# Kernel tuning notes

Hardware: AMD Instinct MI355X
Metric: run time of the kernel (lower is better)

The kernel has to match this reference:

```python
import jax, jax.numpy as jnp
import numpy as np

B, S, I, H = 128, 1024, 512, 1024


def setup_inputs() -> dict:
    key = jax.random.key(0)
    k0, k1, k2, k3, k4, k5 = jax.random.split(key, 6)
    bound = 1.0 / np.sqrt(H)  # PyTorch LSTMCell init range
    sequence = jax.random.normal(k0, (B, S, I), dtype=jnp.float32)
    input_length = jax.random.randint(k1, (B,), 1, S + 1)  # at least length 1
    W_ih = jax.random.uniform(k2, (4 * H, I), minval=-bound, maxval=bound, dtype=jnp.float32)
    W_hh = jax.random.uniform(k3, (4 * H, H), minval=-bound, maxval=bound, dtype=jnp.float32)
    b_ih = jax.random.uniform(k4, (4 * H,), minval=-bound, maxval=bound, dtype=jnp.float32)
    b_hh = jax.random.uniform(k5, (4 * H,), minval=-bound, maxval=bound, dtype=jnp.float32)
    return {"sequence": sequence, "input_length": input_length,
            "W_ih": W_ih, "W_hh": W_hh, "b_ih": b_ih, "b_hh": b_hh}


def reference(sequence, input_length, W_ih, W_hh, b_ih, b_hh):
    # LSTM acceptor: run LSTMCell over time, return hidden state at t = len-1.
    batch, seq_len, _ = sequence.shape
    hidden = W_hh.shape[1]
    h0 = jnp.zeros((batch, hidden), sequence.dtype)
    c0 = jnp.zeros((batch, hidden), sequence.dtype)
    last0 = jnp.zeros((batch, hidden), sequence.dtype)
    last_step = input_length - 1  # [B]

    def step(carry, xs):
        h, c, last = carry
        x_t, t = xs  # x_t: [B, I]
        gates = x_t @ W_ih.T + b_ih + h @ W_hh.T + b_hh  # [B, 4H]
        i_g, f_g, g_g, o_g = jnp.split(gates, 4, axis=-1)  # PyTorch order i,f,g,o
        c = jax.nn.sigmoid(f_g) * c + jax.nn.sigmoid(i_g) * jnp.tanh(g_g)
        h = jax.nn.sigmoid(o_g) * jnp.tanh(c)
        last = jnp.where((t == last_step)[:, None], h, last)
        return (h, c, last), None

    xs = (jnp.swapaxes(sequence, 0, 1), jnp.arange(seq_len, dtype=input_length.dtype))
    (h, c, last), _ = jax.lax.scan(step, (h0, c0, last0), xs)
    return last
```

## Files before the change

### kernel.cpp

```cpp
#include <hip/hip_runtime.h>
#include <hip/hip_bf16.h>
#include <math.h>

#define B_   128
#define S_   1024
#define I_   512
#define H_   1024
#define KC   1536
#define NWG  256
#define NTHR 512
#define LDA  1544

typedef __bf16 v8bf __attribute__((ext_vector_type(8)));
typedef float  v4f  __attribute__((ext_vector_type(4)));

__device__ __forceinline__ v8bf cvt8(const float4 a, const float4 b) {
    v8bf r;
    r[0] = (__bf16)a.x; r[1] = (__bf16)a.y; r[2] = (__bf16)a.z; r[3] = (__bf16)a.w;
    r[4] = (__bf16)b.x; r[5] = (__bf16)b.y; r[6] = (__bf16)b.z; r[7] = (__bf16)b.w;
    return r;
}

__device__ __forceinline__ float sigm(float x) { return 1.f / (1.f + __expf(-x)); }
__device__ __forceinline__ float tanh_fast(float x) {
    const float xc = fminf(fmaxf(x, -15.f), 15.f);
    const float e  = __expf(2.f * xc);
    return (e - 1.f) / (e + 1.f);
}

__global__ void lstm_pack(const float* __restrict__ Wih, const float* __restrict__ Whh,
                          __bf16* __restrict__ Wc)
{
    const size_t e = ((size_t)blockIdx.x * 256 + threadIdx.x) * 8;
    const int col = (int)(e / KC);
    const int k   = (int)(e % KC);
    const float4* src = (k < I_) ? (const float4*)&Wih[(size_t)col * I_ + k]
                                 : (const float4*)&Whh[(size_t)col * H_ + (k - I_)];
    const float4 a = src[0], b = src[1];
    *(v8bf*)&Wc[e] = cvt8(a, b);
}

__global__ __launch_bounds__(NTHR, 1) void lstm_persist(
    const float* __restrict__ seq, const int* __restrict__ len,
    const __bf16* __restrict__ Wc,
    const float* __restrict__ bih, const float* __restrict__ bhh,
    float* __restrict__ out, __bf16* __restrict__ hA, __bf16* __restrict__ hB,
    unsigned* __restrict__ cnt)
{
    __shared__ __bf16 Apan[16 * LDA];
    __shared__ float  glds[4][2][16][33];

    const int wg   = blockIdx.x;
    const int bg   = wg & 7;
    const int cg   = wg >> 3;
    const int tid  = threadIdx.x;
    const int lane = tid & 63;
    const int wv   = tid >> 6;
    const int l15  = lane & 15;
    const int q    = lane >> 4;
    const int gate = wv >> 1;
    const int ks   = wv & 1;

    const int n0   = gate * H_ + cg * 32;
    const int col0 = n0 + l15;
    const int col1 = n0 + 16 + l15;

    v8bf wx0[8], wx1[8], wh0[16], wh1[16];
    {
        const __bf16* wr0 = Wc + (size_t)col0 * KC;
        const __bf16* wr1 = Wc + (size_t)col1 * KC;
        const int xo = ks * 256 + q * 8;
        const int ho = I_ + ks * 512 + q * 8;
        #pragma unroll
        for (int j = 0; j < 8; ++j) {
            wx0[j] = *(const v8bf*)(wr0 + xo + j * 32);
            wx1[j] = *(const v8bf*)(wr1 + xo + j * 32);
        }
        #pragma unroll
        for (int j = 0; j < 16; ++j) {
            wh0[j] = *(const v8bf*)(wr0 + ho + j * 32);
            wh1[j] = *(const v8bf*)(wr1 + ho + j * 32);
        }
        #pragma unroll
        for (int j = 0; j < 8; ++j)
            asm volatile("" : "+v"(wx0[j]), "+v"(wx1[j]));
        #pragma unroll
        for (int j = 0; j < 16; ++j)
            asm volatile("" : "+v"(wh0[j]), "+v"(wh1[j]));
    }
    const float b0 = ks ? 0.f : (bih[col0] + bhh[col0]);
    const float b1 = ks ? 0.f : (bih[col1] + bhh[col1]);

    const int cb = tid >> 5;
    const int cc = tid & 31;
    const int gb = bg * 16 + cb;
    const int gc = cg * 32 + cc;
    const int mylen = len[gb];
    float creg = 0.f;

    for (int t = 0; t < S_; ++t) {
        const __bf16* hrd = (t & 1) ? hA : hB;
        __bf16*       hwr = (t & 1) ? hB : hA;

        {
            const float4* xp = (const float4*)&seq[((size_t)gb * S_ + (size_t)t) * I_ + cc * 16];
            v8bf* dx = (v8bf*)&Apan[cb * LDA + cc * 16];
            const float4 x0 = xp[0], x1 = xp[1];
            dx[0] = cvt8(x0, x1);
            const float4 x2 = xp[2], x3 = xp[3];
            dx[1] = cvt8(x2, x3);
        }

        if (t > 0 && tid == 0) {
            const unsigned* c0 = cnt + ((size_t)(t - 1) * 4) * 32 + bg;
            unsigned s;
            do {
                s  = __hip_atomic_load(c0 +  0, __ATOMIC_RELAXED, __HIP_MEMORY_SCOPE_AGENT);
                s += __hip_atomic_load(c0 + 32, __ATOMIC_RELAXED, __HIP_MEMORY_SCOPE_AGENT);
                s += __hip_atomic_load(c0 + 64, __ATOMIC_RELAXED, __HIP_MEMORY_SCOPE_AGENT);
                s += __hip_atomic_load(c0 + 96, __ATOMIC_RELAXED, __HIP_MEMORY_SCOPE_AGENT);
            } while (s < 32u);
        }
        __syncthreads();

        unsigned long long hv8[8];
        {
            const unsigned long long* hs =
                (const unsigned long long*)(hrd + (size_t)(bg * 16) * H_);
            #pragma unroll
            for (int j = 0; j < 8; ++j)
                hv8[j] = __hip_atomic_load(&hs[cb * 256 + cc + 32 * j],
                                           __ATOMIC_RELAXED, __HIP_MEMORY_SCOPE_AGENT);
        }

        v4f acc0 = {0.f, 0.f, 0.f, 0.f};
        v4f acc1 = {0.f, 0.f, 0.f, 0.f};
        {
            const __bf16* ap = &Apan[l15 * LDA + ks * 256 + q * 8];
            #pragma unroll
            for (int j = 0; j < 8; ++j) {
                const v8bf a = *(const v8bf*)(ap + j * 32);
                acc0 = __builtin_amdgcn_mfma_f32_16x16x32_bf16(a, wx0[j], acc0, 0, 0, 0);
                acc1 = __builtin_amdgcn_mfma_f32_16x16x32_bf16(a, wx1[j], acc1, 0, 0, 0);
            }
        }

        #pragma unroll
        for (int j = 0; j < 8; ++j)
            *(unsigned long long*)&Apan[cb * LDA + I_ + 4 * (cc + 32 * j)] = hv8[j];
        __syncthreads();

        {
            const __bf16* ap = &Apan[l15 * LDA + I_ + ks * 512 + q * 8];
            #pragma unroll
            for (int j = 0; j < 16; ++j) {
                const v8bf a = *(const v8bf*)(ap + j * 32);
                acc0 = __builtin_amdgcn_mfma_f32_16x16x32_bf16(a, wh0[j], acc0, 0, 0, 0);
                acc1 = __builtin_amdgcn_mfma_f32_16x16x32_bf16(a, wh1[j], acc1, 0, 0, 0);
            }
        }

        #pragma unroll
        for (int r = 0; r < 4; ++r) {
            glds[gate][ks][q * 4 + r][l15]      = acc0[r] + b0;
            glds[gate][ks][q * 4 + r][16 + l15] = acc1[r] + b1;
        }
        __syncthreads();

        const float ig = glds[0][0][cb][cc] + glds[0][1][cb][cc];
        const float fg = glds[1][0][cb][cc] + glds[1][1][cb][cc];
        const float gg = glds[2][0][cb][cc] + glds[2][1][cb][cc];
        const float og = glds[3][0][cb][cc] + glds[3][1][cb][cc];

        const float cn = sigm(fg) * creg + sigm(ig) * tanh_fast(gg);
        const float hv = sigm(og) * tanh_fast(cn);
        creg = cn;

        const __bf16 hb = (__bf16)hv;
        const unsigned short us = __builtin_bit_cast(unsigned short, hb);
        const unsigned nb = __shfl_xor((unsigned)us, 1);
        if ((lane & 1) == 0) {
            const unsigned pair = (unsigned)us | (nb << 16);
            __hip_atomic_store((unsigned*)&hwr[(size_t)gb * H_ + gc], pair,
                               __ATOMIC_RELAXED, __HIP_MEMORY_SCOPE_AGENT);
        }
        if (t == mylen - 1) out[(size_t)gb * H_ + gc] = hv;

        __syncthreads();
        if (tid == 0)
            __hip_atomic_fetch_add(cnt + ((size_t)t * 4 + (cg & 3)) * 32 + bg, 1u,
                                   __ATOMIC_RELAXED, __HIP_MEMORY_SCOPE_AGENT);
    }
}

extern "C" void kernel_launch(void* const* d_in, const int* in_sizes, int n_in,
                              void* d_out, int out_size, void* d_ws, size_t ws_size,
                              hipStream_t stream) {
    const float* seq = (const float*)d_in[0];
    const int*   len = (const int*)d_in[1];
    const float* Wih = (const float*)d_in[2];
    const float* Whh = (const float*)d_in[3];
    const float* bih = (const float*)d_in[4];
    const float* bhh = (const float*)d_in[5];
    float* out = (float*)d_out;

    char* ws = (char*)d_ws;
    __bf16*   Wc  = (__bf16*)ws;
    __bf16*   hA  = (__bf16*)(ws + 12582912);
    __bf16*   hB  = (__bf16*)(ws + 12845056);
    unsigned* cnt = (unsigned*)(ws + 13107200);

    hipMemsetAsync(hA, 0, 2 * (size_t)B_ * H_ * sizeof(__bf16), stream);
    hipMemsetAsync(cnt, 0, (size_t)S_ * 4 * 32 * sizeof(unsigned), stream);

    lstm_pack<<<dim3(3072), dim3(256), 0, stream>>>(Wih, Whh, Wc);

    void* args[] = {(void*)&seq, (void*)&len, (void*)&Wc, (void*)&bih,
                    (void*)&bhh, (void*)&out, (void*)&hA, (void*)&hB, (void*)&cnt};
    hipError_t e = hipLaunchCooperativeKernel((void*)lstm_persist, dim3(NWG),
                                              dim3(NTHR), args, 0, stream);
    if (e != hipSuccess) {
        lstm_persist<<<dim3(NWG), dim3(NTHR), 0, stream>>>(seq, len, Wc, bih,
                                                           bhh, out, hA, hB, cnt);
    }
}
```

Measured before the change: 3.348 ms.

## Retile persistent LSTM to 32 batch rows by 16 columns and prefetch next x

Each workgroup now covers 32 batch rows and 16 hidden columns per gate instead of 16 by 32. The grid becomes 4 batch groups by 64 column groups, and the per-step barrier counters grow to 8 slots. Each weight register fragment now feeds two MFMAs over two row halves, which halves the weight registers per wave. The next step's input row is prefetched into a double-buffered LDS panel and overlaps with the recurrent MFMAs, taking the x load off the critical path. In exchange each workgroup reads twice as much h from global memory per step, and the barrier wait now polls 64 arrivals from 8 counters.

```diff
diff --git a/kernel.cpp b/kernel.cpp
--- a/kernel.cpp
+++ b/kernel.cpp
@@ -9,10 +9,12 @@
 #define KC   1536
 #define NWG  256
 #define NTHR 512
-#define LDA  1544
+#define XLD  528
+#define HLD  1040
 
 typedef __bf16 v8bf __attribute__((ext_vector_type(8)));
 typedef float  v4f  __attribute__((ext_vector_type(4)));
+typedef unsigned long long ull;
 
 __device__ __forceinline__ v8bf cvt8(const float4 a, const float4 b) {
     v8bf r;
@@ -47,148 +49,163 @@
     float* __restrict__ out, __bf16* __restrict__ hA, __bf16* __restrict__ hB,
     unsigned* __restrict__ cnt)
 {
-    __shared__ __bf16 Apan[16 * LDA];
-    __shared__ float  glds[4][2][16][33];
+    __shared__ __bf16 xpan[2][32 * XLD];
+    __shared__ __bf16 hpan[32 * HLD];
+    __shared__ float  glds[4][2][32][18];
 
     const int wg   = blockIdx.x;
-    const int bg   = wg & 7;
-    const int cg   = wg >> 3;
+    const int bg   = wg & 3;
+    const int cg   = wg >> 2;
     const int tid  = threadIdx.x;
     const int lane = tid & 63;
     const int wv   = tid >> 6;
     const int l15  = lane & 15;
     const int q    = lane >> 4;
-    const int gate = wv >> 1;
+    const int g    = wv >> 1;
     const int ks   = wv & 1;
 
-    const int n0   = gate * H_ + cg * 32;
-    const int col0 = n0 + l15;
-    const int col1 = n0 + 16 + l15;
-
-    v8bf wx0[8], wx1[8], wh0[16], wh1[16];
+    const int col = g * H_ + cg * 16 + l15;
+
+    v8bf w[24];
     {
-        const __bf16* wr0 = Wc + (size_t)col0 * KC;
-        const __bf16* wr1 = Wc + (size_t)col1 * KC;
-        const int xo = ks * 256 + q * 8;
-        const int ho = I_ + ks * 512 + q * 8;
-        #pragma unroll
-        for (int j = 0; j < 8; ++j) {
-            wx0[j] = *(const v8bf*)(wr0 + xo + j * 32);
-            wx1[j] = *(const v8bf*)(wr1 + xo + j * 32);
-        }
-        #pragma unroll
-        for (int j = 0; j < 16; ++j) {
-            wh0[j] = *(const v8bf*)(wr0 + ho + j * 32);
-            wh1[j] = *(const v8bf*)(wr1 + ho + j * 32);
-        }
+        const __bf16* wr = Wc + (size_t)col * KC;
         #pragma unroll
         for (int j = 0; j < 8; ++j)
-            asm volatile("" : "+v"(wx0[j]), "+v"(wx1[j]));
+            w[j] = *(const v8bf*)(wr + ks * 256 + q * 8 + j * 32);
         #pragma unroll
         for (int j = 0; j < 16; ++j)
-            asm volatile("" : "+v"(wh0[j]), "+v"(wh1[j]));
-    }
-    const float b0 = ks ? 0.f : (bih[col0] + bhh[col0]);
-    const float b1 = ks ? 0.f : (bih[col1] + bhh[col1]);
-
-    const int cb = tid >> 5;
-    const int cc = tid & 31;
-    const int gb = bg * 16 + cb;
-    const int gc = cg * 32 + cc;
+            w[8 + j] = *(const v8bf*)(wr + I_ + ks * 512 + q * 8 + j * 32);
+        #pragma unroll
+        for (int j = 0; j < 24; ++j) asm volatile("" : "+v"(w[j]));
+    }
+    const float b0 = ks ? 0.f : (bih[col] + bhh[col]);
+
+    const int cb  = tid >> 4;
+    const int ccc = tid & 15;
+    const int gb  = bg * 32 + cb;
+    const int gc  = cg * 16 + ccc;
     const int mylen = len[gb];
     float creg = 0.f;
 
+    const float* xrow = seq + (size_t)gb * (S_ * I_);
+
+    {
+        const float4* xs = (const float4*)xrow;
+        #pragma unroll
+        for (int jj = 0; jj < 4; ++jj) {
+            const int fi = 2 * ccc + 32 * jj;
+            const float4 a = xs[fi], b = xs[fi + 1];
+            *(v8bf*)&xpan[0][cb * XLD + fi * 4] = cvt8(a, b);
+        }
+    }
+
     for (int t = 0; t < S_; ++t) {
+        const int buf = t & 1;
         const __bf16* hrd = (t & 1) ? hA : hB;
         __bf16*       hwr = (t & 1) ? hB : hA;
 
-        {
-            const float4* xp = (const float4*)&seq[((size_t)gb * S_ + (size_t)t) * I_ + cc * 16];
-            v8bf* dx = (v8bf*)&Apan[cb * LDA + cc * 16];
-            const float4 x0 = xp[0], x1 = xp[1];
-            dx[0] = cvt8(x0, x1);
-            const float4 x2 = xp[2], x3 = xp[3];
-            dx[1] = cvt8(x2, x3);
-        }
-
         if (t > 0 && tid == 0) {
-            const unsigned* c0 = cnt + ((size_t)(t - 1) * 4) * 32 + bg;
+            const unsigned* c0 = cnt + ((size_t)(t - 1) * 8) * 32 + bg;
             unsigned s;
             do {
-                s  = __hip_atomic_load(c0 +  0, __ATOMIC_RELAXED, __HIP_MEMORY_SCOPE_AGENT);
-                s += __hip_atomic_load(c0 + 32, __ATOMIC_RELAXED, __HIP_MEMORY_SCOPE_AGENT);
-                s += __hip_atomic_load(c0 + 64, __ATOMIC_RELAXED, __HIP_MEMORY_SCOPE_AGENT);
-                s += __hip_atomic_load(c0 + 96, __ATOMIC_RELAXED, __HIP_MEMORY_SCOPE_AGENT);
-            } while (s < 32u);
-        }
-        __syncthreads();
-
-        unsigned long long hv8[8];
+                s = 0;
+                #pragma unroll
+                for (int u = 0; u < 8; ++u)
+                    s += __hip_atomic_load(c0 + u * 32, __ATOMIC_RELAXED,
+                                           __HIP_MEMORY_SCOPE_AGENT);
+            } while (s < 64u);
+        }
+        __syncthreads();
+
+        ull hv[16];
         {
-            const unsigned long long* hs =
-                (const unsigned long long*)(hrd + (size_t)(bg * 16) * H_);
-            #pragma unroll
-            for (int j = 0; j < 8; ++j)
-                hv8[j] = __hip_atomic_load(&hs[cb * 256 + cc + 32 * j],
-                                           __ATOMIC_RELAXED, __HIP_MEMORY_SCOPE_AGENT);
+            const ull* hs = (const ull*)(hrd + (size_t)(bg * 32) * H_);
+            #pragma unroll
+            for (int j = 0; j < 16; ++j)
+                hv[j] = __hip_atomic_load(&hs[cb * 256 + ccc + 16 * j],
+                                          __ATOMIC_RELAXED, __HIP_MEMORY_SCOPE_AGENT);
         }
 
         v4f acc0 = {0.f, 0.f, 0.f, 0.f};
         v4f acc1 = {0.f, 0.f, 0.f, 0.f};
         {
-            const __bf16* ap = &Apan[l15 * LDA + ks * 256 + q * 8];
+            const __bf16* ap0 = &xpan[buf][l15 * XLD + ks * 256 + q * 8];
+            const __bf16* ap1 = ap0 + 16 * XLD;
             #pragma unroll
             for (int j = 0; j < 8; ++j) {
-                const v8bf a = *(const v8bf*)(ap + j * 32);
-                acc0 = __builtin_amdgcn_mfma_f32_16x16x32_bf16(a, wx0[j], acc0, 0, 0, 0);
-                acc1 = __builtin_amdgcn_mfma_f32_16x16x32_bf16(a, wx1[j], acc1, 0, 0, 0);
-            }
-        }
-
-        #pragma unroll
-        for (int j = 0; j < 8; ++j)
-            *(unsigned long long*)&Apan[cb * LDA + I_ + 4 * (cc + 32 * j)] = hv8[j];
-        __syncthreads();
+                acc0 = __builtin_amdgcn_mfma_f32_16x16x32_bf16(
+                           *(const v8bf*)(ap0 + j * 32), w[j], acc0, 0, 0, 0);
+                acc1 = __builtin_amdgcn_mfma_f32_16x16x32_bf16(
+                           *(const v8bf*)(ap1 + j * 32), w[j], acc1, 0, 0, 0);
+            }
+        }
+
+        #pragma unroll
+        for (int j = 0; j < 16; ++j)
+            *(ull*)&hpan[cb * HLD + 4 * (ccc + 16 * j)] = hv[j];
+        __syncthreads();
+
+        float4 xf[8];
+        const bool pf = (t + 1 < S_);
+        if (pf) {
+            const float4* xs = (const float4*)(xrow + (size_t)(t + 1) * I_);
+            #pragma unroll
+            for (int jj = 0; jj < 4; ++jj) {
+                const int fi = 2 * ccc + 32 * jj;
+                xf[2 * jj]     = xs[fi];
+                xf[2 * jj + 1] = xs[fi + 1];
+            }
+        }
 
         {
-            const __bf16* ap = &Apan[l15 * LDA + I_ + ks * 512 + q * 8];
+            const __bf16* ap0 = &hpan[l15 * HLD + ks * 512 + q * 8];
+            const __bf16* ap1 = ap0 + 16 * HLD;
             #pragma unroll
             for (int j = 0; j < 16; ++j) {
-                const v8bf a = *(const v8bf*)(ap + j * 32);
-                acc0 = __builtin_amdgcn_mfma_f32_16x16x32_bf16(a, wh0[j], acc0, 0, 0, 0);
-                acc1 = __builtin_amdgcn_mfma_f32_16x16x32_bf16(a, wh1[j], acc1, 0, 0, 0);
+                acc0 = __builtin_amdgcn_mfma_f32_16x16x32_bf16(
+                           *(const v8bf*)(ap0 + j * 32), w[8 + j], acc0, 0, 0, 0);
+                acc1 = __builtin_amdgcn_mfma_f32_16x16x32_bf16(
+                           *(const v8bf*)(ap1 + j * 32), w[8 + j], acc1, 0, 0, 0);
+            }
+        }
+
+        if (pf) {
+            #pragma unroll
+            for (int jj = 0; jj < 4; ++jj) {
+                const int fi = 2 * ccc + 32 * jj;
+                *(v8bf*)&xpan[buf ^ 1][cb * XLD + fi * 4] =
+                    cvt8(xf[2 * jj], xf[2 * jj + 1]);
             }
         }
 
         #pragma unroll
         for (int r = 0; r < 4; ++r) {
-            glds[gate][ks][q * 4 + r][l15]      = acc0[r] + b0;
-            glds[gate][ks][q * 4 + r][16 + l15] = acc1[r] + b1;
-        }
-        __syncthreads();
-
-        const float ig = glds[0][0][cb][cc] + glds[0][1][cb][cc];
-        const float fg = glds[1][0][cb][cc] + glds[1][1][cb][cc];
-        const float gg = glds[2][0][cb][cc] + glds[2][1][cb][cc];
-        const float og = glds[3][0][cb][cc] + glds[3][1][cb][cc];
+            glds[g][ks][q * 4 + r][l15]      = acc0[r] + b0;
+            glds[g][ks][16 + q * 4 + r][l15] = acc1[r] + b0;
+        }
+        __syncthreads();
+
+        const float ig = glds[0][0][cb][ccc] + glds[0][1][cb][ccc];
+        const float fg = glds[1][0][cb][ccc] + glds[1][1][cb][ccc];
+        const float gg = glds[2][0][cb][ccc] + glds[2][1][cb][ccc];
+        const float og = glds[3][0][cb][ccc] + glds[3][1][cb][ccc];
 
         const float cn = sigm(fg) * creg + sigm(ig) * tanh_fast(gg);
-        const float hv = sigm(og) * tanh_fast(cn);
+        const float hvv = sigm(og) * tanh_fast(cn);
         creg = cn;
 
-        const __bf16 hb = (__bf16)hv;
-        const unsigned short us = __builtin_bit_cast(unsigned short, hb);
+        const unsigned short us = __builtin_bit_cast(unsigned short, (__bf16)hvv);
         const unsigned nb = __shfl_xor((unsigned)us, 1);
-        if ((lane & 1) == 0) {
+        if (!(tid & 1)) {
             const unsigned pair = (unsigned)us | (nb << 16);
             __hip_atomic_store((unsigned*)&hwr[(size_t)gb * H_ + gc], pair,
                                __ATOMIC_RELAXED, __HIP_MEMORY_SCOPE_AGENT);
         }
-        if (t == mylen - 1) out[(size_t)gb * H_ + gc] = hv;
+        if (t == mylen - 1) out[(size_t)gb * H_ + gc] = hvv;
 
         __syncthreads();
         if (tid == 0)
-            __hip_atomic_fetch_add(cnt + ((size_t)t * 4 + (cg & 3)) * 32 + bg, 1u,
+            __hip_atomic_fetch_add(cnt + ((size_t)t * 8 + (cg & 7)) * 32 + bg, 1u,
                                    __ATOMIC_RELAXED, __HIP_MEMORY_SCOPE_AGENT);
     }
 }
@@ -211,7 +228,7 @@
     unsigned* cnt = (unsigned*)(ws + 13107200);
 
     hipMemsetAsync(hA, 0, 2 * (size_t)B_ * H_ * sizeof(__bf16), stream);
-    hipMemsetAsync(cnt, 0, (size_t)S_ * 4 * 32 * sizeof(unsigned), stream);
+    hipMemsetAsync(cnt, 0, (size_t)S_ * 8 * 32 * sizeof(unsigned), stream);
 
     lstm_pack<<<dim3(3072), dim3(256), 0, stream>>>(Wih, Whh, Wc);
 
```

New measurement: 5.913 ms. 1.77x slower.
